# Kernel tuning notes

Measured on AMD Instinct MI355X. Metric: run time of the kernel, lower is better.

Reference implementation:

```python
import jax, jax.numpy as jnp
import numpy as np

N = 50000      # nodes
E = 800000     # edges
F_IN = 128     # num_features
H = 64         # hidden_dim
NE = 3         # num_experts
G = 64         # graphs in batch
NC = 3         # num_classes
EPS = 1e-5


def setup_inputs() -> dict:
    key = jax.random.key(0)
    ks = jax.random.split(key, 10)
    def w(k, shape, fan):
        return (jax.random.normal(k, shape, jnp.float32) / np.sqrt(fan)).astype(jnp.float32)
    return dict(
        x=jax.random.normal(ks[0], (N, F_IN), jnp.float32),
        edge_index=jax.random.randint(ks[1], (2, E), 0, N),
        batch=jnp.sort(jax.random.randint(ks[2], (N,), 0, G)),
        W_exp=w(ks[3], (NE, F_IN, H), F_IN), b_exp=jnp.zeros((NE, H), jnp.float32),
        gate_W1=w(ks[4], (F_IN, H // 2), F_IN), gate_b1=jnp.zeros((H // 2,), jnp.float32),
        gate_W2=w(ks[5], (H // 2, NE), H // 2), gate_b2=jnp.zeros((NE,), jnp.float32),
        W2=w(ks[6], (H, H), H), b2=jnp.zeros((H,), jnp.float32),
        bn1_g=jnp.ones((H,), jnp.float32), bn1_b=jnp.zeros((H,), jnp.float32),
        bn2_g=jnp.ones((H,), jnp.float32), bn2_b=jnp.zeros((H,), jnp.float32),
        cls_W=w(ks[7], (3 * H, NC), 3 * H), cls_b=jnp.zeros((NC,), jnp.float32),
    )


def _gcn_prop(h, src, dst, deg_isqrt, deg_inv):
    # GCN propagation with self-loops: out_i = sum_{j->i} d_j^-1/2 d_i^-1/2 h_j + d_i^-1 h_i
    bshape = (-1,) + (1,) * (h.ndim - 1)
    norm = (deg_isqrt[src] * deg_isqrt[dst]).reshape(bshape)
    agg = jax.ops.segment_sum(h[src] * norm, dst, num_segments=N)
    return agg + h * deg_inv.reshape(bshape)


def _bn(h, g, b):
    # training-mode batch norm over the node dimension (biased variance)
    mu = h.mean(0)
    var = h.var(0)
    return (h - mu) * jax.lax.rsqrt(var + EPS) * g + b


def reference(x, edge_index, batch, W_exp, b_exp, gate_W1, gate_b1, gate_W2, gate_b2,
              W2, b2, bn1_g, bn1_b, bn2_g, bn2_b, cls_W, cls_b):
    src, dst = edge_index[0], edge_index[1]
    deg = jax.ops.segment_sum(jnp.ones((E,), jnp.float32), dst, num_segments=N) + 1.0
    deg_isqrt = jax.lax.rsqrt(deg)
    deg_inv = 1.0 / deg

    # gating network: softmax over experts, per node
    gate = jax.nn.softmax(jnp.maximum(x @ gate_W1 + gate_b1, 0.0) @ gate_W2 + gate_b2, axis=1)  # [N, NE]

    # all experts vectorized: transform then propagate [N, NE, H]
    h = jnp.einsum('nf,efh->neh', x, W_exp)
    h = _gcn_prop(h, src, dst, deg_isqrt, deg_inv) + b_exp
    h = jnp.einsum('ne,neh->nh', gate, h)  # gated combine

    h = jnp.maximum(_bn(h, bn1_g, bn1_b), 0.0)
    # dropout is identity in eval mode
    h = _gcn_prop(h @ W2, src, dst, deg_isqrt, deg_inv) + b2
    h = jnp.maximum(_bn(h, bn2_g, bn2_b), 0.0)

    cnt = jax.ops.segment_sum(jnp.ones((N,), jnp.float32), batch, num_segments=G)
    x_sum = jax.ops.segment_sum(h, batch, num_segments=G)
    x_mean = x_sum / jnp.maximum(cnt, 1.0)[:, None]
    x_max = jax.ops.segment_max(h, batch, num_segments=G)
    z = jnp.concatenate([x_mean, x_max, x_sum], axis=1)  # [G, 3H]
    return z @ cls_W + cls_b
```

## Files before the change

### kernel.cpp

```cpp
#include <hip/hip_runtime.h>

#define N_NODES 50000
#define N_EDGES 800000
#define F 128
#define HDIM 64
#define NE 3
#define NGRAPH 64
#define NC 3
#define BN_EPS 1e-5f
#define NBLK_A 200
#define NBUCK 196
#define NBLK_EXP 782
#define NBLK_GY 1563

typedef __attribute__((ext_vector_type(8))) short short8;
typedef __attribute__((ext_vector_type(4))) float f32x4;

__device__ inline unsigned short f2bf(float f) {
    unsigned int u = __float_as_uint(f);
    unsigned int r = (u + 0x7FFFu + ((u >> 16) & 1u)) >> 16;
    return (unsigned short)r;
}
__device__ inline float bf2f(unsigned short u) {
    return __uint_as_float(((unsigned int)u) << 16);
}

__global__ __launch_bounds__(256) void k_prep(const float* __restrict__ Wexp,
        const float* __restrict__ gW1, const int* __restrict__ batch,
        const int* __restrict__ dst,
        unsigned short* __restrict__ wpack, unsigned short* __restrict__ gwpack,
        int* __restrict__ gstart, int* __restrict__ bh, float* __restrict__ zbase) {
    int b = blockIdx.x, tid = threadIdx.x;
    if (b < 12) {
        int t0 = b * 256 + tid;
        int f = t0 >> 6, l = t0 & 63;
        int e = f >> 4, t = (f >> 2) & 3, kk = f & 3;
        int h = t * 16 + (l & 15);
        int kbase = kk * 32 + (l >> 4) * 8;
        short8 o;
        #pragma unroll
        for (int j = 0; j < 8; ++j)
            o[j] = (short)f2bf(Wexp[e * (F * HDIM) + (kbase + j) * HDIM + h]);
        ((short8*)wpack)[f * 64 + l] = o;
    } else if (b == 12) {
        for (int t0 = tid; t0 < 8 * 64; t0 += 256) {
            int f = t0 >> 6, l = t0 & 63;
            int t = f >> 2, kk = f & 3;
            int h = t * 16 + (l & 15);
            int kbase = kk * 32 + (l >> 4) * 8;
            short8 o;
            #pragma unroll
            for (int j = 0; j < 8; ++j)
                o[j] = (short)f2bf(gW1[(kbase + j) * 32 + h]);
            ((short8*)gwpack)[f * 64 + l] = o;
        }
    } else if (b == 13) {
        int g = tid;
        if (g <= NGRAPH) {
            int lo = 0, hi = N_NODES;
            while (lo < hi) { int m = (lo + hi) >> 1; if (batch[m] < g) lo = m + 1; else hi = m; }
            gstart[g] = lo;
        }
    } else if (b < 14 + NBLK_A) {
        __shared__ int hist[256];
        hist[tid] = 0;
        __syncthreads();
        int base = (b - 14) * 4000;
        for (int i = tid; i < 4000; i += 256)
            atomicAdd(&hist[dst[base + i] >> 8], 1);
        __syncthreads();
        bh[(b - 14) * 256 + tid] = hist[tid];
    } else {
        int idx = (b - 14 - NBLK_A) * 256 + tid;
        if (idx < 8192) zbase[idx] = 0.f;
    }
}

__global__ __launch_bounds__(256) void k_bscan(int* __restrict__ bh, int* __restrict__ bucketbase,
                                               int* __restrict__ row_start) {
    int b = threadIdx.x;
    int sum = 0;
    #pragma unroll 4
    for (int k = 0; k < NBLK_A; ++k) {
        int v = bh[k * 256 + b];
        bh[k * 256 + b] = sum;
        sum += v;
    }
    int lane = b & 63, wid = b >> 6;
    __shared__ int wsums[4];
    int xsc = sum;
    #pragma unroll
    for (int off = 1; off < 64; off <<= 1) {
        int u = __shfl_up(xsc, off, 64);
        if (lane >= off) xsc += u;
    }
    if (lane == 63) wsums[wid] = xsc;
    __syncthreads();
    int woff = 0;
    for (int wq = 0; wq < wid; ++wq) woff += wsums[wq];
    int excl = woff + xsc - sum;
    bucketbase[b] = excl;
    if (b == 255) {
        bucketbase[256] = excl + sum;
        row_start[N_NODES] = excl + sum;
    }
}

__global__ __launch_bounds__(256) void k_bplace(const int* __restrict__ ei, const int* __restrict__ bh,
        const int* __restrict__ bucketbase, int2* __restrict__ pairs) {
    __shared__ int cur[256];
    int tid = threadIdx.x;
    cur[tid] = bucketbase[tid] + bh[blockIdx.x * 256 + tid];
    __syncthreads();
    int base = blockIdx.x * 4000;
    for (int i = tid; i < 4000; i += 256) {
        int e = base + i;
        int s = ei[e], d = ei[N_EDGES + e];
        int slot = atomicAdd(&cur[d >> 8], 1);
        pairs[slot] = make_int2(s, d);
    }
}

__global__ __launch_bounds__(256) void k_bfinal(const int2* __restrict__ pairs,
        const int* __restrict__ bucketbase, int* __restrict__ row_start,
        float* __restrict__ deg_isqrt, int* __restrict__ csr_src) {
    __shared__ int deg[256];
    __shared__ int cur[256];
    __shared__ int wsums[4];
    int b = blockIdx.x, t = threadIdx.x;
    int beg = bucketbase[b], end = bucketbase[b + 1];
    deg[t] = 0;
    __syncthreads();
    for (int i = beg + t; i < end; i += 256)
        atomicAdd(&deg[pairs[i].y & 255], 1);
    __syncthreads();
    int d = deg[t];
    int lane = t & 63, wid = t >> 6;
    int xsc = d;
    #pragma unroll
    for (int off = 1; off < 64; off <<= 1) {
        int u = __shfl_up(xsc, off, 64);
        if (lane >= off) xsc += u;
    }
    if (lane == 63) wsums[wid] = xsc;
    __syncthreads();
    int woff = 0;
    for (int wq = 0; wq < wid; ++wq) woff += wsums[wq];
    int rs = beg + woff + xsc - d;
    int node = b * 256 + t;
    if (node < N_NODES) {
        row_start[node] = rs;
        deg_isqrt[node] = rsqrtf((float)d + 1.0f);
    }
    cur[t] = rs;
    __syncthreads();
    for (int i = beg + t; i < end; i += 256) {
        int2 p = pairs[i];
        int slot = atomicAdd(&cur[p.y & 255], 1);
        csr_src[slot] = p.x;
    }
}

__global__ __launch_bounds__(256) void k_gateM(const float* __restrict__ x,
        const float* __restrict__ deg_isqrt, const unsigned short* __restrict__ gwpack,
        const float* __restrict__ gb1, const float* __restrict__ gW2,
        const float* __restrict__ gb2, float* __restrict__ gate,
        unsigned short* __restrict__ xpb1) {
    int tid = threadIdx.x;
    int w = tid >> 6, l = tid & 63;
    int lo = l & 15, hi = l >> 4;
    int n0 = blockIdx.x * 64 + w * 16;
    int nlo = n0 + lo;
    bool vrow = nlo < N_NODES;
    int arow = vrow ? nlo : N_NODES - 1;
    float si = deg_isqrt[arow];
    short8 a[4];
    #pragma unroll
    for (int kk = 0; kk < 4; ++kk) {
        int c4 = (kk * 32 + hi * 8) >> 2;
        float4 v0 = ((const float4*)x)[(size_t)arow * 32 + c4];
        float4 v1 = ((const float4*)x)[(size_t)arow * 32 + c4 + 1];
        short8 t8;
        t8[0] = (short)f2bf(v0.x); t8[1] = (short)f2bf(v0.y);
        t8[2] = (short)f2bf(v0.z); t8[3] = (short)f2bf(v0.w);
        t8[4] = (short)f2bf(v1.x); t8[5] = (short)f2bf(v1.y);
        t8[6] = (short)f2bf(v1.z); t8[7] = (short)f2bf(v1.w);
        a[kk] = t8;
        if (vrow) {
            ushort4 o0, o1;
            o0.x = f2bf(v0.x * si); o0.y = f2bf(v0.y * si);
            o0.z = f2bf(v0.z * si); o0.w = f2bf(v0.w * si);
            o1.x = f2bf(v1.x * si); o1.y = f2bf(v1.y * si);
            o1.z = f2bf(v1.z * si); o1.w = f2bf(v1.w * si);
            ((ushort4*)xpb1)[(size_t)arow * 32 + c4]     = o0;
            ((ushort4*)xpb1)[(size_t)arow * 32 + c4 + 1] = o1;
        }
    }
    const short8* gw8 = (const short8*)gwpack;
    f32x4 acc0 = {0.f, 0.f, 0.f, 0.f}, acc1 = {0.f, 0.f, 0.f, 0.f};
    #pragma unroll
    for (int kk = 0; kk < 4; ++kk) {
        acc0 = __builtin_amdgcn_mfma_f32_16x16x32_bf16(a[kk], gw8[kk * 64 + l], acc0, 0, 0, 0);
        acc1 = __builtin_amdgcn_mfma_f32_16x16x32_bf16(a[kk], gw8[(4 + kk) * 64 + l], acc1, 0, 0, 0);
    }
    float b1a = gb1[lo], b1b = gb1[16 + lo];
    float w20[3], w21[3];
    #pragma unroll
    for (int e = 0; e < 3; ++e) { w20[e] = gW2[lo * 3 + e]; w21[e] = gW2[(16 + lo) * 3 + e]; }
    float bb0 = gb2[0], bb1 = gb2[1], bb2 = gb2[2];
    #pragma unroll
    for (int r = 0; r < 4; ++r) {
        float h0 = fmaxf(acc0[r] + b1a, 0.f);
        float h1 = fmaxf(acc1[r] + b1b, 0.f);
        float le[3];
        #pragma unroll
        for (int e = 0; e < 3; ++e) {
            float p = fmaf(h0, w20[e], h1 * w21[e]);
            p += __shfl_xor(p, 1, 64);
            p += __shfl_xor(p, 2, 64);
            p += __shfl_xor(p, 4, 64);
            p += __shfl_xor(p, 8, 64);
            le[e] = p;
        }
        le[0] += bb0; le[1] += bb1; le[2] += bb2;
        float m = fmaxf(le[0], fmaxf(le[1], le[2]));
        float e0 = __expf(le[0] - m), e1 = __expf(le[1] - m), e2 = __expf(le[2] - m);
        float inv = 1.f / (e0 + e1 + e2);
        int n = n0 + hi * 4 + r;
        if (n < N_NODES && lo < 3) {
            float gg = (lo == 0) ? e0 * inv : (lo == 1 ? e1 * inv : e2 * inv);
            gate[n * 3 + lo] = gg;
        }
    }
}

__global__ __launch_bounds__(256) void k_gsum_x(const int* __restrict__ csr_src,
        const int* __restrict__ row_start, const float* __restrict__ deg_isqrt,
        const unsigned short* __restrict__ hin, unsigned short* __restrict__ out) {
    int lane = threadIdx.x & 15;
    int grp  = threadIdx.x >> 4;
    int n = blockIdx.x * 16 + grp;
    if (n >= N_NODES) return;
    const short8* h8 = (const short8*)hin;
    int beg = row_start[n], end = row_start[n + 1];
    short8 sv = h8[(size_t)n * 16 + lane];
    float a[8];
    #pragma unroll
    for (int j = 0; j < 8; ++j) a[j] = bf2f((unsigned short)sv[j]);
    int e = beg;
    for (; e + 3 < end; e += 4) {
        int s0 = csr_src[e], s1 = csr_src[e + 1], s2 = csr_src[e + 2], s3 = csr_src[e + 3];
        short8 v0 = h8[(size_t)s0 * 16 + lane];
        short8 v1 = h8[(size_t)s1 * 16 + lane];
        short8 v2 = h8[(size_t)s2 * 16 + lane];
        short8 v3 = h8[(size_t)s3 * 16 + lane];
        #pragma unroll
        for (int j = 0; j < 8; ++j)
            a[j] += (bf2f((unsigned short)v0[j]) + bf2f((unsigned short)v1[j]))
                  + (bf2f((unsigned short)v2[j]) + bf2f((unsigned short)v3[j]));
    }
    for (; e < end; ++e) {
        short8 v0 = h8[(size_t)csr_src[e] * 16 + lane];
        #pragma unroll
        for (int j = 0; j < 8; ++j) a[j] += bf2f((unsigned short)v0[j]);
    }
    float s = deg_isqrt[n];
    short8 o;
    #pragma unroll
    for (int j = 0; j < 8; ++j) o[j] = (short)f2bf(a[j] * s);
    ((short8*)out)[(size_t)n * 16 + lane] = o;
}

__global__ __launch_bounds__(256) void k_expert(const unsigned short* __restrict__ xp,
        const unsigned short* __restrict__ wpack, const float* __restrict__ bexp,
        const float* __restrict__ gate, unsigned short* __restrict__ h1preb,
        float* __restrict__ partial1) {
    int tid = threadIdx.x;
    int w = tid >> 6, l = tid & 63;
    int n0 = blockIdx.x * 64 + w * 16;
    int lo = l & 15, hi = l >> 4;
    int arow = n0 + lo; if (arow >= N_NODES) arow = N_NODES - 1;
    const short8* xr = (const short8*)xp + (size_t)arow * 16;
    short8 a0 = xr[hi], a1 = xr[4 + hi], a2 = xr[8 + hi], a3 = xr[12 + hi];
    const short8* wp8 = (const short8*)wpack;
    float comb[4][4];
    #pragma unroll
    for (int t = 0; t < 4; ++t)
        #pragma unroll
        for (int r = 0; r < 4; ++r) comb[t][r] = 0.f;
    int nrow[4];
    #pragma unroll
    for (int r = 0; r < 4; ++r) {
        int n = n0 + hi * 4 + r;
        nrow[r] = (n < N_NODES) ? n : -1;
    }
    #pragma unroll
    for (int e = 0; e < NE; ++e) {
        float g_[4];
        #pragma unroll
        for (int r = 0; r < 4; ++r) g_[r] = (nrow[r] >= 0) ? gate[nrow[r] * 3 + e] : 0.f;
        #pragma unroll
        for (int t = 0; t < 4; ++t) {
            int fbase = (e * 16 + t * 4) * 64 + l;
            f32x4 acc = {0.f, 0.f, 0.f, 0.f};
            acc = __builtin_amdgcn_mfma_f32_16x16x32_bf16(a0, wp8[fbase      ], acc, 0, 0, 0);
            acc = __builtin_amdgcn_mfma_f32_16x16x32_bf16(a1, wp8[fbase +  64], acc, 0, 0, 0);
            acc = __builtin_amdgcn_mfma_f32_16x16x32_bf16(a2, wp8[fbase + 128], acc, 0, 0, 0);
            acc = __builtin_amdgcn_mfma_f32_16x16x32_bf16(a3, wp8[fbase + 192], acc, 0, 0, 0);
            float be = bexp[e * HDIM + t * 16 + lo];
            #pragma unroll
            for (int r = 0; r < 4; ++r) comb[t][r] = fmaf(g_[r], acc[r] + be, comb[t][r]);
        }
    }
    __shared__ float sred[4][128];
    #pragma unroll
    for (int t = 0; t < 4; ++t) {
        float s = 0.f, q = 0.f;
        #pragma unroll
        for (int r = 0; r < 4; ++r) {
            if (nrow[r] >= 0) {
                float v = comb[t][r];
                h1preb[(size_t)nrow[r] * HDIM + t * 16 + lo] = f2bf(v);
                s += v; q = fmaf(v, v, q);
            }
        }
        s += __shfl_xor(s, 16, 64); s += __shfl_xor(s, 32, 64);
        q += __shfl_xor(q, 16, 64); q += __shfl_xor(q, 32, 64);
        if (hi == 0) {
            sred[w][t * 16 + lo] = s;
            sred[w][64 + t * 16 + lo] = q;
        }
    }
    __syncthreads();
    if (tid < 128)
        partial1[blockIdx.x * 128 + tid] =
            sred[0][tid] + sred[1][tid] + sred[2][tid] + sred[3][tid];
}

__global__ __launch_bounds__(256) void k_colred(const float* __restrict__ partial, int nblk,
                                                float* __restrict__ sums) {
    int c = blockIdx.x;
    int tid = threadIdx.x;
    float s = 0.f;
    for (int k = tid; k < nblk; k += 256)
        s += partial[(size_t)k * 128 + c];
    __shared__ float red[256];
    red[tid] = s;
    __syncthreads();
    #pragma unroll
    for (int off = 128; off >= 1; off >>= 1) {
        if (tid < off) red[tid] += red[tid + off];
        __syncthreads();
    }
    if (tid == 0) sums[c] = red[0];
}

__global__ __launch_bounds__(256) void k_w2(const unsigned short* __restrict__ h1preb,
        const float* __restrict__ sums, const float* __restrict__ bng, const float* __restrict__ bnb,
        const float* __restrict__ W2, const float* __restrict__ deg_isqrt,
        unsigned short* __restrict__ y) {
    __shared__ float scsh_s[128];
    __shared__ float4 hsd[64 * 16];
    __shared__ float  wsd[64 * 64];
    int tid = threadIdx.x;
    if (tid < 64) {
        float mu = sums[tid] * (1.0f / N_NODES);
        float var = sums[64 + tid] * (1.0f / N_NODES) - mu * mu;
        float rs = rsqrtf(var + BN_EPS);
        float sc = rs * bng[tid];
        scsh_s[tid] = sc;
        scsh_s[64 + tid] = bnb[tid] - mu * sc;
    }
    int nbase = blockIdx.x * 64;
    for (int i = tid; i < 64 * 16; i += 256) ((float4*)wsd)[i] = ((const float4*)W2)[i];
    __syncthreads();
    for (int i = tid; i < 64 * 8; i += 256) {
        int r = i >> 3, c8 = i & 7;
        int n = nbase + r; if (n >= N_NODES) n = N_NODES - 1;
        short8 v8 = ((const short8*)h1preb)[(size_t)n * 8 + c8];
        float vv[8];
        #pragma unroll
        for (int j = 0; j < 8; ++j) {
            int col = c8 * 8 + j;
            vv[j] = fmaxf(fmaf(bf2f((unsigned short)v8[j]), scsh_s[col], scsh_s[64 + col]), 0.f);
        }
        hsd[r * 16 + c8 * 2]     = make_float4(vv[0], vv[1], vv[2], vv[3]);
        hsd[r * 16 + c8 * 2 + 1] = make_float4(vv[4], vv[5], vv[6], vv[7]);
    }
    __syncthreads();
    int h = tid & 63, iq = tid >> 6;
    float acc[16];
    #pragma unroll
    for (int i = 0; i < 16; ++i) acc[i] = 0.f;
    for (int k4 = 0; k4 < 16; ++k4) {
        float w0 = wsd[(k4 * 4 + 0) * 64 + h];
        float w1 = wsd[(k4 * 4 + 1) * 64 + h];
        float w2v = wsd[(k4 * 4 + 2) * 64 + h];
        float w3 = wsd[(k4 * 4 + 3) * 64 + h];
        #pragma unroll
        for (int i = 0; i < 16; ++i) {
            float4 xv = hsd[(iq * 16 + i) * 16 + k4];
            acc[i] = fmaf(xv.x, w0, acc[i]);
            acc[i] = fmaf(xv.y, w1, acc[i]);
            acc[i] = fmaf(xv.z, w2v, acc[i]);
            acc[i] = fmaf(xv.w, w3, acc[i]);
        }
    }
    #pragma unroll
    for (int i = 0; i < 16; ++i) {
        int n = nbase + iq * 16 + i;
        if (n < N_NODES) y[(size_t)n * 64 + h] = f2bf(acc[i] * deg_isqrt[n]);
    }
}

__global__ __launch_bounds__(256) void k_gsum_y(const int* __restrict__ csr_src,
        const int* __restrict__ row_start, const float* __restrict__ deg_isqrt,
        const unsigned short* __restrict__ hin, unsigned short* __restrict__ out,
        float* __restrict__ partial2) {
    int tid = threadIdx.x;
    int lane8 = tid & 7;
    int grp = tid >> 3;
    int n = blockIdx.x * 32 + grp;
    bool valid = n < N_NODES;
    int nn = valid ? n : N_NODES - 1;
    const short8* h8 = (const short8*)hin;
    int beg = row_start[nn], end = row_start[nn + 1];
    short8 sv = h8[(size_t)nn * 8 + lane8];
    float a[8];
    #pragma unroll
    for (int j = 0; j < 8; ++j) a[j] = bf2f((unsigned short)sv[j]);
    int e = beg;
    for (; e + 3 < end; e += 4) {
        int s0 = csr_src[e], s1 = csr_src[e + 1], s2 = csr_src[e + 2], s3 = csr_src[e + 3];
        short8 v0 = h8[(size_t)s0 * 8 + lane8];
        short8 v1 = h8[(size_t)s1 * 8 + lane8];
        short8 v2 = h8[(size_t)s2 * 8 + lane8];
        short8 v3 = h8[(size_t)s3 * 8 + lane8];
        #pragma unroll
        for (int j = 0; j < 8; ++j)
            a[j] += (bf2f((unsigned short)v0[j]) + bf2f((unsigned short)v1[j]))
                  + (bf2f((unsigned short)v2[j]) + bf2f((unsigned short)v3[j]));
    }
    for (; e < end; ++e) {
        short8 v0 = h8[(size_t)csr_src[e] * 8 + lane8];
        #pragma unroll
        for (int j = 0; j < 8; ++j) a[j] += bf2f((unsigned short)v0[j]);
    }
    float s = deg_isqrt[nn];
    float o[8];
    #pragma unroll
    for (int j = 0; j < 8; ++j) o[j] = a[j] * s;
    if (valid) {
        short8 ob;
        #pragma unroll
        for (int j = 0; j < 8; ++j) ob[j] = (short)f2bf(o[j]);
        ((short8*)out)[(size_t)n * 8 + lane8] = ob;
    }
    float ss[8], sq[8];
    #pragma unroll
    for (int j = 0; j < 8; ++j) {
        float v = valid ? o[j] : 0.f;
        ss[j] = v; sq[j] = v * v;
    }
    #pragma unroll
    for (int j = 0; j < 8; ++j) {
        ss[j] += __shfl_xor(ss[j], 8, 64);  sq[j] += __shfl_xor(sq[j], 8, 64);
        ss[j] += __shfl_xor(ss[j], 16, 64); sq[j] += __shfl_xor(sq[j], 16, 64);
        ss[j] += __shfl_xor(ss[j], 32, 64); sq[j] += __shfl_xor(sq[j], 32, 64);
    }
    __shared__ float sred[4][128];
    int wv = tid >> 6;
    if (((tid >> 3) & 7) == 0) {
        #pragma unroll
        for (int j = 0; j < 8; ++j) {
            sred[wv][lane8 * 8 + j] = ss[j];
            sred[wv][64 + lane8 * 8 + j] = sq[j];
        }
    }
    __syncthreads();
    if (tid < 128)
        partial2[blockIdx.x * 128 + tid] =
            sred[0][tid] + sred[1][tid] + sred[2][tid] + sred[3][tid];
}

__global__ __launch_bounds__(256) void k_pool(const unsigned short* __restrict__ xp2b,
        const float* __restrict__ sums, const float* __restrict__ bng, const float* __restrict__ bnb,
        const int* __restrict__ gstart,
        float* __restrict__ psum, unsigned int* __restrict__ pmax) {
    __shared__ float scsh_s[128];
    int tid = threadIdx.x;
    if (tid < 64) {
        float mu = sums[tid] * (1.0f / N_NODES);
        float var = sums[64 + tid] * (1.0f / N_NODES) - mu * mu;
        float rs = rsqrtf(var + BN_EPS);
        float sc = rs * bng[tid];
        scsh_s[tid] = sc;
        scsh_s[64 + tid] = bnb[tid] - mu * sc;
    }
    __syncthreads();
    int g = blockIdx.x >> 2, ck = blockIdx.x & 3;
    int h = tid & 63, q = tid >> 6;
    int s0 = gstart[g], s1 = gstart[g + 1];
    int len = s1 - s0;
    int cbeg = s0 + (len * ck) / 4;
    int cend = s0 + (len * (ck + 1)) / 4;
    float sc = scsh_s[h], sh = scsh_s[64 + h];
    float ls = 0.f, lm = 0.f;
    int r = cbeg + q;
    for (; r + 12 < cend; r += 16) {
        float v0 = fmaxf(fmaf(bf2f(xp2b[(size_t)r * 64 + h]), sc, sh), 0.f);
        float v1 = fmaxf(fmaf(bf2f(xp2b[(size_t)(r + 4) * 64 + h]), sc, sh), 0.f);
        float v2 = fmaxf(fmaf(bf2f(xp2b[(size_t)(r + 8) * 64 + h]), sc, sh), 0.f);
        float v3 = fmaxf(fmaf(bf2f(xp2b[(size_t)(r + 12) * 64 + h]), sc, sh), 0.f);
        ls += (v0 + v1) + (v2 + v3);
        lm = fmaxf(fmaxf(fmaxf(lm, v0), fmaxf(v1, v2)), v3);
    }
    for (; r < cend; r += 4) {
        float v = fmaxf(fmaf(bf2f(xp2b[(size_t)r * 64 + h]), sc, sh), 0.f);
        ls += v; lm = fmaxf(lm, v);
    }
    __shared__ float red[2][4][64];
    red[0][q][h] = ls; red[1][q][h] = lm;
    __syncthreads();
    if (q == 0) {
        ls = red[0][0][h] + red[0][1][h] + red[0][2][h] + red[0][3][h];
        lm = fmaxf(fmaxf(red[1][0][h], red[1][1][h]), fmaxf(red[1][2][h], red[1][3][h]));
        atomicAdd(&psum[g * 64 + h], ls);
        atomicMax(&pmax[g * 64 + h], __float_as_uint(lm));
    }
}

__global__ void k_cls(const float* __restrict__ psum, const unsigned int* __restrict__ pmax,
                      const int* __restrict__ gstart, const float* __restrict__ Wc,
                      const float* __restrict__ bc, float* __restrict__ out) {
    int t = threadIdx.x;
    if (t >= NGRAPH * NC) return;
    int g = t / NC, c = t % NC;
    float cnt = (float)(gstart[g + 1] - gstart[g]);
    float invc = 1.f / fmaxf(cnt, 1.f);
    float acc = bc[c];
    #pragma unroll 8
    for (int j = 0; j < 64; ++j) {
        float s = psum[g * 64 + j];
        float mx = __uint_as_float(pmax[g * 64 + j]);
        acc = fmaf(s * invc, Wc[j * 3 + c], acc);
        acc = fmaf(mx, Wc[(64 + j) * 3 + c], acc);
        acc = fmaf(s, Wc[(128 + j) * 3 + c], acc);
    }
    out[g * NC + c] = acc;
}

extern "C" void kernel_launch(void* const* d_in, const int* in_sizes, int n_in,
                              void* d_out, int out_size, void* d_ws, size_t ws_size,
                              hipStream_t stream) {
    const float* x    = (const float*)d_in[0];
    const int*   ei   = (const int*)d_in[1];
    const int*   batch= (const int*)d_in[2];
    const float* Wexp = (const float*)d_in[3];
    const float* bexp = (const float*)d_in[4];
    const float* gW1  = (const float*)d_in[5];
    const float* gb1  = (const float*)d_in[6];
    const float* gW2  = (const float*)d_in[7];
    const float* gb2  = (const float*)d_in[8];
    const float* W2   = (const float*)d_in[9];
    const float* bn1g = (const float*)d_in[11];
    const float* bn1b = (const float*)d_in[12];
    const float* bn2g = (const float*)d_in[13];
    const float* bn2b = (const float*)d_in[14];
    const float* clsW = (const float*)d_in[15];
    const float* clsb = (const float*)d_in[16];
    float* out = (float*)d_out;

    float* ws = (float*)d_ws;
    const size_t NN = N_NODES;
    float* deg_isqrt = ws;
    float* gate      = ws + NN;
    unsigned short* xpb1   = (unsigned short*)(ws + 4 * NN);
    unsigned short* xpb    = (unsigned short*)(ws + 68 * NN);
    unsigned short* h1preb = (unsigned short*)(ws + 132 * NN);
    unsigned short* ypb    = (unsigned short*)(ws + 164 * NN);
    unsigned short* xp2b   = (unsigned short*)(ws + 196 * NN);
    float* stats     = ws + 260 * NN;
    float* sums1 = stats + 256;
    float* sums2 = stats + 384;
    float* psum  = stats + 512;
    unsigned int* pmax = (unsigned int*)(stats + 512 + 4096);
    int* gstart  = (int*)(stats + 512 + 8192);
    float* partial1 = stats + 16384;
    float* partial2 = partial1 + 131072;
    int* row_start  = (int*)(partial2 + 262144);
    int* bh         = row_start + NN + 8;
    int* bucketbase = bh + NBLK_A * 256;
    int* csr_src    = bucketbase + 264;
    int2* pairs     = (int2*)(csr_src + N_EDGES);
    unsigned short* wpack  = (unsigned short*)(pairs + N_EDGES);
    unsigned short* gwpack = wpack + 24576;

    k_prep<<<14 + NBLK_A + 32, 256, 0, stream>>>(Wexp, gW1, batch, ei + N_EDGES,
                                                 wpack, gwpack, gstart, bh, psum);
    k_bscan<<<1, 256, 0, stream>>>(bh, bucketbase, row_start);
    k_bplace<<<NBLK_A, 256, 0, stream>>>(ei, bh, bucketbase, pairs);
    k_bfinal<<<NBUCK, 256, 0, stream>>>(pairs, bucketbase, row_start, deg_isqrt, csr_src);

    k_gateM<<<NBLK_EXP, 256, 0, stream>>>(x, deg_isqrt, gwpack, gb1, gW2, gb2, gate, xpb1);
    k_gsum_x<<<(N_NODES + 15) / 16, 256, 0, stream>>>(csr_src, row_start, deg_isqrt, xpb1, xpb);
    k_expert<<<NBLK_EXP, 256, 0, stream>>>(xpb, wpack, bexp, gate, h1preb, partial1);
    k_colred<<<128, 256, 0, stream>>>(partial1, NBLK_EXP, sums1);
    k_w2<<<NBLK_EXP, 256, 0, stream>>>(h1preb, sums1, bn1g, bn1b, W2, deg_isqrt, ypb);
    k_gsum_y<<<NBLK_GY, 256, 0, stream>>>(csr_src, row_start, deg_isqrt, ypb, xp2b, partial2);
    k_colred<<<128, 256, 0, stream>>>(partial2, NBLK_GY, sums2);
    k_pool<<<NGRAPH * 4, 256, 0, stream>>>(xp2b, sums2, bn2g, bn2b, gstart, psum, pmax);
    k_cls<<<1, 256, 0, stream>>>(psum, pmax, gstart, clsW, clsb, out);
}
```

Baseline: 158.4 us.

## Fuse first-layer gather-sum into expert MFMA kernel and pack edge pairs

Merges the first-layer neighbor aggregation (k_gsum_x) into the expert MFMA kernel. Each block now gathers its 64 rows into XOR-swizzled shared memory and feeds them straight to the MFMAs, so the intermediate xpb buffer is no longer written to and read back from global memory, and one launch is removed. Separately, edge (src,dst) pairs in the CSR build are packed into one int (src<<8 | dst&255), which halves the pairs traffic. The cost is that the gather now runs with only 782 blocks, each looping over four row groups, so parallelism and latency hiding during the gather are reduced.

```diff
diff --git a/kernel.cpp b/kernel.cpp
--- a/kernel.cpp
+++ b/kernel.cpp
@@ -107,7 +107,7 @@
 }
 
 __global__ __launch_bounds__(256) void k_bplace(const int* __restrict__ ei, const int* __restrict__ bh,
-        const int* __restrict__ bucketbase, int2* __restrict__ pairs) {
+        const int* __restrict__ bucketbase, int* __restrict__ pairs) {
     __shared__ int cur[256];
     int tid = threadIdx.x;
     cur[tid] = bucketbase[tid] + bh[blockIdx.x * 256 + tid];
@@ -117,11 +117,11 @@
         int e = base + i;
         int s = ei[e], d = ei[N_EDGES + e];
         int slot = atomicAdd(&cur[d >> 8], 1);
-        pairs[slot] = make_int2(s, d);
-    }
-}
-
-__global__ __launch_bounds__(256) void k_bfinal(const int2* __restrict__ pairs,
+        pairs[slot] = (s << 8) | (d & 255);
+    }
+}
+
+__global__ __launch_bounds__(256) void k_bfinal(const int* __restrict__ pairs,
         const int* __restrict__ bucketbase, int* __restrict__ row_start,
         float* __restrict__ deg_isqrt, int* __restrict__ csr_src) {
     __shared__ int deg[256];
@@ -132,7 +132,7 @@
     deg[t] = 0;
     __syncthreads();
     for (int i = beg + t; i < end; i += 256)
-        atomicAdd(&deg[pairs[i].y & 255], 1);
+        atomicAdd(&deg[pairs[i] & 255], 1);
     __syncthreads();
     int d = deg[t];
     int lane = t & 63, wid = t >> 6;
@@ -155,9 +155,9 @@
     cur[t] = rs;
     __syncthreads();
     for (int i = beg + t; i < end; i += 256) {
-        int2 p = pairs[i];
-        int slot = atomicAdd(&cur[p.y & 255], 1);
-        csr_src[slot] = p.x;
+        int p = pairs[i];
+        int slot = atomicAdd(&cur[p & 255], 1);
+        csr_src[slot] = p >> 8;
     }
 }
 
@@ -234,54 +234,60 @@
     }
 }
 
-__global__ __launch_bounds__(256) void k_gsum_x(const int* __restrict__ csr_src,
+__global__ __launch_bounds__(256) void k_gx_exp(const int* __restrict__ csr_src,
         const int* __restrict__ row_start, const float* __restrict__ deg_isqrt,
-        const unsigned short* __restrict__ hin, unsigned short* __restrict__ out) {
-    int lane = threadIdx.x & 15;
-    int grp  = threadIdx.x >> 4;
-    int n = blockIdx.x * 16 + grp;
-    if (n >= N_NODES) return;
-    const short8* h8 = (const short8*)hin;
-    int beg = row_start[n], end = row_start[n + 1];
-    short8 sv = h8[(size_t)n * 16 + lane];
-    float a[8];
-    #pragma unroll
-    for (int j = 0; j < 8; ++j) a[j] = bf2f((unsigned short)sv[j]);
-    int e = beg;
-    for (; e + 3 < end; e += 4) {
-        int s0 = csr_src[e], s1 = csr_src[e + 1], s2 = csr_src[e + 2], s3 = csr_src[e + 3];
-        short8 v0 = h8[(size_t)s0 * 16 + lane];
-        short8 v1 = h8[(size_t)s1 * 16 + lane];
-        short8 v2 = h8[(size_t)s2 * 16 + lane];
-        short8 v3 = h8[(size_t)s3 * 16 + lane];
-        #pragma unroll
-        for (int j = 0; j < 8; ++j)
-            a[j] += (bf2f((unsigned short)v0[j]) + bf2f((unsigned short)v1[j]))
-                  + (bf2f((unsigned short)v2[j]) + bf2f((unsigned short)v3[j]));
-    }
-    for (; e < end; ++e) {
-        short8 v0 = h8[(size_t)csr_src[e] * 16 + lane];
-        #pragma unroll
-        for (int j = 0; j < 8; ++j) a[j] += bf2f((unsigned short)v0[j]);
-    }
-    float s = deg_isqrt[n];
-    short8 o;
-    #pragma unroll
-    for (int j = 0; j < 8; ++j) o[j] = (short)f2bf(a[j] * s);
-    ((short8*)out)[(size_t)n * 16 + lane] = o;
-}
-
-__global__ __launch_bounds__(256) void k_expert(const unsigned short* __restrict__ xp,
+        const unsigned short* __restrict__ xpb1,
         const unsigned short* __restrict__ wpack, const float* __restrict__ bexp,
         const float* __restrict__ gate, unsigned short* __restrict__ h1preb,
         float* __restrict__ partial1) {
+    __shared__ short8 xls[64][16];
+    __shared__ float sred[4][128];
     int tid = threadIdx.x;
+    int nbase = blockIdx.x * 64;
+    const short8* h8 = (const short8*)xpb1;
+    {
+        int lane = tid & 15, grp = tid >> 4;
+        for (int it = 0; it < 4; ++it) {
+            int row = it * 16 + grp;
+            int n = nbase + row; if (n >= N_NODES) n = N_NODES - 1;
+            int beg = row_start[n], end = row_start[n + 1];
+            short8 sv = h8[(size_t)n * 16 + lane];
+            float a[8];
+            #pragma unroll
+            for (int j = 0; j < 8; ++j) a[j] = bf2f((unsigned short)sv[j]);
+            int e = beg;
+            for (; e + 3 < end; e += 4) {
+                int s0 = csr_src[e], s1 = csr_src[e + 1], s2 = csr_src[e + 2], s3 = csr_src[e + 3];
+                short8 v0 = h8[(size_t)s0 * 16 + lane];
+                short8 v1 = h8[(size_t)s1 * 16 + lane];
+                short8 v2 = h8[(size_t)s2 * 16 + lane];
+                short8 v3 = h8[(size_t)s3 * 16 + lane];
+                #pragma unroll
+                for (int j = 0; j < 8; ++j)
+                    a[j] += (bf2f((unsigned short)v0[j]) + bf2f((unsigned short)v1[j]))
+                          + (bf2f((unsigned short)v2[j]) + bf2f((unsigned short)v3[j]));
+            }
+            for (; e < end; ++e) {
+                short8 v0 = h8[(size_t)csr_src[e] * 16 + lane];
+                #pragma unroll
+                for (int j = 0; j < 8; ++j) a[j] += bf2f((unsigned short)v0[j]);
+            }
+            float s = deg_isqrt[n];
+            short8 o;
+            #pragma unroll
+            for (int j = 0; j < 8; ++j) o[j] = (short)f2bf(a[j] * s);
+            xls[row][lane ^ grp] = o;
+        }
+    }
+    __syncthreads();
     int w = tid >> 6, l = tid & 63;
-    int n0 = blockIdx.x * 64 + w * 16;
+    int n0 = nbase + w * 16;
     int lo = l & 15, hi = l >> 4;
-    int arow = n0 + lo; if (arow >= N_NODES) arow = N_NODES - 1;
-    const short8* xr = (const short8*)xp + (size_t)arow * 16;
-    short8 a0 = xr[hi], a1 = xr[4 + hi], a2 = xr[8 + hi], a3 = xr[12 + hi];
+    int row = w * 16 + lo;
+    short8 a0 = xls[row][(hi)      ^ lo];
+    short8 a1 = xls[row][(4 + hi)  ^ lo];
+    short8 a2 = xls[row][(8 + hi)  ^ lo];
+    short8 a3 = xls[row][(12 + hi) ^ lo];
     const short8* wp8 = (const short8*)wpack;
     float comb[4][4];
     #pragma unroll
@@ -312,7 +318,6 @@
             for (int r = 0; r < 4; ++r) comb[t][r] = fmaf(g_[r], acc[r] + be, comb[t][r]);
         }
     }
-    __shared__ float sred[4][128];
     #pragma unroll
     for (int t = 0; t < 4; ++t) {
         float s = 0.f, q = 0.f;
@@ -576,7 +581,6 @@
     float* deg_isqrt = ws;
     float* gate      = ws + NN;
     unsigned short* xpb1   = (unsigned short*)(ws + 4 * NN);
-    unsigned short* xpb    = (unsigned short*)(ws + 68 * NN);
     unsigned short* h1preb = (unsigned short*)(ws + 132 * NN);
     unsigned short* ypb    = (unsigned short*)(ws + 164 * NN);
     unsigned short* xp2b   = (unsigned short*)(ws + 196 * NN);
@@ -592,7 +596,7 @@
     int* bh         = row_start + NN + 8;
     int* bucketbase = bh + NBLK_A * 256;
     int* csr_src    = bucketbase + 264;
-    int2* pairs     = (int2*)(csr_src + N_EDGES);
+    int* pairs      = csr_src + N_EDGES;
     unsigned short* wpack  = (unsigned short*)(pairs + N_EDGES);
     unsigned short* gwpack = wpack + 24576;
 
@@ -603,8 +607,8 @@
     k_bfinal<<<NBUCK, 256, 0, stream>>>(pairs, bucketbase, row_start, deg_isqrt, csr_src);
 
     k_gateM<<<NBLK_EXP, 256, 0, stream>>>(x, deg_isqrt, gwpack, gb1, gW2, gb2, gate, xpb1);
-    k_gsum_x<<<(N_NODES + 15) / 16, 256, 0, stream>>>(csr_src, row_start, deg_isqrt, xpb1, xpb);
-    k_expert<<<NBLK_EXP, 256, 0, stream>>>(xpb, wpack, bexp, gate, h1preb, partial1);
+    k_gx_exp<<<NBLK_EXP, 256, 0, stream>>>(csr_src, row_start, deg_isqrt, xpb1,
+                                           wpack, bexp, gate, h1preb, partial1);
     k_colred<<<128, 256, 0, stream>>>(partial1, NBLK_EXP, sums1);
     k_w2<<<NBLK_EXP, 256, 0, stream>>>(h1preb, sums1, bn1g, bn1b, W2, deg_isqrt, ypb);
     k_gsum_y<<<NBLK_GY, 256, 0, stream>>>(csr_src, row_start, deg_isqrt, ypb, xp2b, partial2);
```

New measurement: 178.8 us. +12.9%, slower.
